# Kernel optimization log

Hardware: AMD Instinct MI355X
Metric: run time of the kernel (lower is better)

The kernel has to match this reference:

```python
import jax, jax.numpy as jnp
import numpy as np
import math

DIM = 256
B, S = 4, 2048


def setup_inputs() -> dict:
    key = jax.random.key(0)
    ks = jax.random.split(key, 8)
    h = DIM // 2
    return {
        "features": jax.random.normal(ks[0], (B, S, DIM), dtype=jnp.float32),
        "W1": jax.random.normal(ks[1], (DIM, h), dtype=jnp.float32) / np.sqrt(DIM),
        "b1": jnp.zeros((h,), dtype=jnp.float32),
        "ln_g": jnp.ones((h,), dtype=jnp.float32),
        "ln_b": jnp.zeros((h,), dtype=jnp.float32),
        "W2": jax.random.normal(ks[2], (h, 1), dtype=jnp.float32) / np.sqrt(h),
        "b2": jnp.zeros((1,), dtype=jnp.float32),
        "target_entropy": jnp.full((1,), math.log(DIM), dtype=jnp.float32),
        "temperature": jnp.ones((1,), dtype=jnp.float32),
    }


def _compute_entropy(features, temperature):
    b, s, d = features.shape
    x = features.reshape(-1, d)  # [N, D]
    sq = jnp.sum(x * x, axis=-1)  # [N]
    # squared euclidean distance (cdist(...)**2), clamped for numerical safety
    d2 = jnp.maximum(sq[:, None] + sq[None, :] - 2.0 * (x @ x.T), 0.0)  # [N, N]
    kernel = jnp.exp(-d2 / (2.0 * temperature[0] ** 2))
    probs = kernel / jnp.sum(kernel, axis=-1, keepdims=True)
    entropy = -jnp.sum(probs * jnp.log(probs + 1e-6), axis=-1)
    return entropy.reshape(b, s)


def _entropy_estimator(features, W1, b1, ln_g, ln_b, W2, b2):
    h = features @ W1 + b1  # [B, S, D/2]
    mu = jnp.mean(h, axis=-1, keepdims=True)
    var = jnp.mean((h - mu) ** 2, axis=-1, keepdims=True)
    hn = (h - mu) / jnp.sqrt(var + 1e-5) * ln_g + ln_b
    hg = jax.nn.gelu(hn, approximate=False)
    return (hg @ W2 + b2).squeeze(-1)  # [B, S]


def reference(features, W1, b1, ln_g, ln_b, W2, b2, target_entropy, temperature):
    current_entropy = _compute_entropy(features, temperature)  # [B, S]
    # estimated_entropy is computed in the original forward but unused in outputs
    _est = _entropy_estimator(features, W1, b1, ln_g, ln_b, W2, b2)
    entropy_diff = current_entropy - target_entropy[0]
    control_signal = jax.nn.sigmoid(-entropy_diff / temperature[0])  # [B, S]
    controlled_features = features * control_signal[..., None]
    return controlled_features, control_signal
```

## Files before the change

### kernel.cpp

```cpp
#include <hip/hip_runtime.h>

#define N 8192
#define D 256
#define BM 128
#define BN 64
#define CH 512
#define NJT (CH / BN)

typedef short short8 __attribute__((ext_vector_type(8)));
typedef float f32x4 __attribute__((ext_vector_type(4)));

__device__ __forceinline__ unsigned short f2bf(float f) {
    unsigned int u = __float_as_uint(f);
    u += 0x7fffu + ((u >> 16) & 1u);
    return (unsigned short)(u >> 16);
}
__device__ __forceinline__ float bf2f(unsigned short h) {
    return __uint_as_float(((unsigned int)h) << 16);
}

#define GLDS16(g, l) __builtin_amdgcn_global_load_lds(                      \
    (const __attribute__((address_space(1))) void*)(g),                     \
    (__attribute__((address_space(3))) void*)(l), 16, 0, 0)

__global__ __launch_bounds__(256) void k_cvt(const float* __restrict__ x,
                                             unsigned short* __restrict__ xb,
                                             float* __restrict__ sq,
                                             float* __restrict__ Sarr,
                                             float* __restrict__ Larr) {
    const int wv = threadIdx.x >> 6, lane = threadIdx.x & 63;
    const int row = blockIdx.x * 4 + wv;
    const float4 v = ((const float4*)x)[(size_t)row * 64 + lane];
    unsigned short pa = f2bf(v.x), pb = f2bf(v.y), pc = f2bf(v.z), pd = f2bf(v.w);
    float a = bf2f(pa), b = bf2f(pb), c = bf2f(pc), d = bf2f(pd);
    float s = a * a + b * b + c * c + d * d;
    ((ushort4*)xb)[(size_t)row * 64 + lane] = make_ushort4(pa, pb, pc, pd);
#pragma unroll
    for (int m = 1; m < 64; m <<= 1) s += __shfl_xor(s, m, 64);
    if (lane == 0) {
        sq[row] = s;
        Sarr[row] = 0.0f;
        Larr[row] = 0.0f;
    }
}

__global__ __launch_bounds__(256, 3) void k_gram(const unsigned short* __restrict__ xb,
                                                 const float* __restrict__ sq,
                                                 const float* __restrict__ temp,
                                                 float* __restrict__ Sarr,
                                                 float* __restrict__ Larr) {
    __shared__ unsigned short Bs[BN * D];

    const int tid = threadIdx.x;
    const int wv = tid >> 6, lane = tid & 63;
    const int q = lane >> 4, c = lane & 15;
    const int rowbase = blockIdx.x * BM;
    const int colbase0 = blockIdx.y * CH;
    const float T = temp[0];
    const float inv2T2 = 1.0f / (2.0f * T * T);

    short8 av[2][8];
#pragma unroll
    for (int tr = 0; tr < 2; ++tr) {
        const unsigned short* ap = xb + (size_t)(rowbase + wv * 32 + tr * 16 + c) * D;
#pragma unroll
        for (int kk = 0; kk < 8; ++kk)
            av[tr][kk] = *(const short8*)(ap + kk * 32 + q * 8);
    }

    float sqr[8];
#pragma unroll
    for (int tr = 0; tr < 2; ++tr)
#pragma unroll
        for (int r = 0; r < 4; ++r)
            sqr[tr * 4 + r] = sq[rowbase + wv * 32 + tr * 16 + q * 4 + r];

    int rofs[4], rx3[4];
#pragma unroll
    for (int tc = 0; tc < 4; ++tc) {
        int r = tc * 16 + c;
        rofs[tc] = r * D;
        rx3[tc] = r & 7;
    }

    const int seg0 = wv * 8;
    const int rhalf = lane >> 5, slot = lane & 31;

    float Sp[8], Lp[8];
#pragma unroll
    for (int i = 0; i < 8; ++i) { Sp[i] = 0.0f; Lp[i] = 0.0f; }

    for (int jt = 0; jt < NJT; ++jt) {
        const int colbase = colbase0 + jt * BN;
        __syncthreads();
#pragma unroll
        for (int i = 0; i < 8; ++i) {
            int seg = seg0 + i;
            int row = seg * 2 + rhalf;
            int g = slot ^ (row & 7);
            GLDS16(xb + (size_t)(colbase + row) * D + g * 8, Bs + seg * 512);
        }
        __syncthreads();

        f32x4 acc[2][4];
#pragma unroll
        for (int tr = 0; tr < 2; ++tr)
#pragma unroll
            for (int tc = 0; tc < 4; ++tc)
#pragma unroll
                for (int r = 0; r < 4; ++r) acc[tr][tc][r] = 0.0f;

#pragma unroll
        for (int kk = 0; kk < 8; ++kk) {
            short8 bv[4];
#pragma unroll
            for (int tc = 0; tc < 4; ++tc)
                bv[tc] = *(const short8*)(Bs + rofs[tc] + (((4 * kk + q) ^ rx3[tc]) << 3));
#pragma unroll
            for (int tr = 0; tr < 2; ++tr)
#pragma unroll
                for (int tc = 0; tc < 4; ++tc)
                    acc[tr][tc] = __builtin_amdgcn_mfma_f32_16x16x32_bf16(
                        av[tr][kk], bv[tc], acc[tr][tc], 0, 0, 0);
        }

        float scq[4];
#pragma unroll
        for (int tc = 0; tc < 4; ++tc) scq[tc] = sq[colbase + tc * 16 + c];

#pragma unroll
        for (int tr = 0; tr < 2; ++tr)
#pragma unroll
            for (int tc = 0; tc < 4; ++tc)
#pragma unroll
                for (int r = 0; r < 4; ++r) {
                    float g = acc[tr][tc][r];
                    float d2 = fmaxf(sqr[tr * 4 + r] + scq[tc] - 2.0f * g, 0.0f);
                    float t = -d2 * inv2T2;
                    float e = __expf(t);
                    Sp[tr * 4 + r] += e;
                    Lp[tr * 4 + r] += e * t;
                }
    }

#pragma unroll
    for (int m = 1; m <= 8; m <<= 1)
#pragma unroll
        for (int i = 0; i < 8; ++i) {
            Sp[i] += __shfl_xor(Sp[i], m, 64);
            Lp[i] += __shfl_xor(Lp[i], m, 64);
        }
    if (c == 0) {
#pragma unroll
        for (int i = 0; i < 8; ++i) {
            int row = rowbase + wv * 32 + (i >> 2) * 16 + q * 4 + (i & 3);
            atomicAdd(&Sarr[row], Sp[i]);
            atomicAdd(&Larr[row], Lp[i]);
        }
    }
}

__global__ __launch_bounds__(256) void k_ctrl(const float* __restrict__ Sarr,
                                              const float* __restrict__ Larr,
                                              const float* __restrict__ target,
                                              const float* __restrict__ temp,
                                              float* __restrict__ ctrl,
                                              float* __restrict__ out) {
    const int r = blockIdx.x * 256 + threadIdx.x;
    float S = Sarr[r], L = Larr[r];
    float H = __logf(S) - L / S;
    float z = (H - target[0]) / temp[0];
    float cs = 1.0f / (1.0f + __expf(z));
    ctrl[r] = cs;
    out[(size_t)N * D + r] = cs;
}

__global__ __launch_bounds__(256) void k_scale(const float* __restrict__ x,
                                               const float* __restrict__ ctrl,
                                               float* __restrict__ out) {
    const size_t i = (size_t)blockIdx.x * 256 + threadIdx.x;
    float4 v = ((const float4*)x)[i];
    float cs = ctrl[i >> 6];
    float4 o;
    o.x = v.x * cs; o.y = v.y * cs; o.z = v.z * cs; o.w = v.w * cs;
    ((float4*)out)[i] = o;
}

extern "C" void kernel_launch(void* const* d_in, const int* in_sizes, int n_in,
                              void* d_out, int out_size, void* d_ws, size_t ws_size,
                              hipStream_t stream) {
    const float* x = (const float*)d_in[0];
    const float* target = (const float*)d_in[7];
    const float* temp = (const float*)d_in[8];
    float* out = (float*)d_out;

    float* wsf = (float*)d_ws;
    float* sq = wsf;
    float* Sarr = wsf + N;
    float* Larr = wsf + 2 * N;
    float* ctrl = wsf + 3 * N;

    const size_t need = 4 * (size_t)N * sizeof(float) + (size_t)N * D * sizeof(unsigned short);
    unsigned short* xb = (ws_size >= need) ? (unsigned short*)(wsf + 4 * N)
                                           : (unsigned short*)d_out;

    k_cvt<<<N / 4, 256, 0, stream>>>(x, xb, sq, Sarr, Larr);
    k_gram<<<dim3(N / BM, N / CH), 256, 0, stream>>>(xb, sq, temp, Sarr, Larr);
    k_ctrl<<<N / 256, 256, 0, stream>>>(Sarr, Larr, target, temp, ctrl, out);
    k_scale<<<(N * (D / 4)) / 256, 256, 0, stream>>>(x, ctrl, out);
}
```

Before: 126.1 us.

## Exploit Gram matrix symmetry with upper-triangular tiles and fuse control/scale kernels

Uses the symmetry of the pairwise distance matrix by launching only the upper-triangular 128x128 tile pairs (2080 blocks). Each exp value is accumulated into both the row and the column entropy sums, with column sums sent via extra atomics. This roughly halves the MFMA and exp work, at the cost of more registers, lower occupancy (launch bounds go from 3 to 2) and extra atomic traffic. The control and scale kernels are also merged into one, so the ctrl buffer and one launch go away.

```diff
diff --git a/kernel.cpp b/kernel.cpp
--- a/kernel.cpp
+++ b/kernel.cpp
@@ -3,9 +3,6 @@
 #define N 8192
 #define D 256
 #define BM 128
-#define BN 64
-#define CH 512
-#define NJT (CH / BN)
 
 typedef short short8 __attribute__((ext_vector_type(8)));
 typedef float f32x4 __attribute__((ext_vector_type(4)));
@@ -44,64 +41,65 @@
     }
 }
 
-__global__ __launch_bounds__(256, 3) void k_gram(const unsigned short* __restrict__ xb,
+__global__ __launch_bounds__(256, 2) void k_gram(const unsigned short* __restrict__ xb,
                                                  const float* __restrict__ sq,
                                                  const float* __restrict__ temp,
                                                  float* __restrict__ Sarr,
                                                  float* __restrict__ Larr) {
-    __shared__ unsigned short Bs[BN * D];
+    __shared__ unsigned short Bs[BM * D];
 
     const int tid = threadIdx.x;
     const int wv = tid >> 6, lane = tid & 63;
-    const int q = lane >> 4, c = lane & 15;
-    const int rowbase = blockIdx.x * BM;
-    const int colbase0 = blockIdx.y * CH;
+    const int q8 = lane >> 4, c = lane & 15;
+
+    const int b = blockIdx.x;
+    int p = (int)((129.0f - sqrtf(16641.0f - 8.0f * (float)b)) * 0.5f);
+    while (64 * p - (p * (p - 1)) / 2 > b) --p;
+    while (64 * (p + 1) - ((p + 1) * p) / 2 <= b) ++p;
+    const int qblk = p + (b - (64 * p - (p * (p - 1)) / 2));
+    const int rowbase = p * BM, colbase = qblk * BM;
+
+    const int rhalf = lane >> 5, slot = lane & 31;
+#pragma unroll
+    for (int i = 0; i < 16; ++i) {
+        int seg = wv * 16 + i;
+        int row = seg * 2 + rhalf;
+        int g = slot ^ (row & 7);
+        GLDS16(xb + (size_t)(colbase + row) * D + g * 8, Bs + seg * 512);
+    }
+
+    short8 av[2][8];
+#pragma unroll
+    for (int tr = 0; tr < 2; ++tr) {
+        const unsigned short* ap = xb + (size_t)(rowbase + wv * 32 + tr * 16 + c) * D;
+#pragma unroll
+        for (int kk = 0; kk < 8; ++kk)
+            av[tr][kk] = *(const short8*)(ap + kk * 32 + q8 * 8);
+    }
+
+    float sqr[8];
+#pragma unroll
+    for (int tr = 0; tr < 2; ++tr)
+#pragma unroll
+        for (int r = 0; r < 4; ++r)
+            sqr[tr * 4 + r] = sq[rowbase + wv * 32 + tr * 16 + q8 * 4 + r];
+    float scq[8];
+#pragma unroll
+    for (int i = 0; i < 8; ++i)
+        scq[i] = sq[colbase + (i >> 2) * 64 + (i & 3) * 16 + c];
+
     const float T = temp[0];
     const float inv2T2 = 1.0f / (2.0f * T * T);
-
-    short8 av[2][8];
-#pragma unroll
-    for (int tr = 0; tr < 2; ++tr) {
-        const unsigned short* ap = xb + (size_t)(rowbase + wv * 32 + tr * 16 + c) * D;
-#pragma unroll
-        for (int kk = 0; kk < 8; ++kk)
-            av[tr][kk] = *(const short8*)(ap + kk * 32 + q * 8);
-    }
-
-    float sqr[8];
-#pragma unroll
-    for (int tr = 0; tr < 2; ++tr)
-#pragma unroll
-        for (int r = 0; r < 4; ++r)
-            sqr[tr * 4 + r] = sq[rowbase + wv * 32 + tr * 16 + q * 4 + r];
-
-    int rofs[4], rx3[4];
-#pragma unroll
-    for (int tc = 0; tc < 4; ++tc) {
-        int r = tc * 16 + c;
-        rofs[tc] = r * D;
-        rx3[tc] = r & 7;
-    }
-
-    const int seg0 = wv * 8;
-    const int rhalf = lane >> 5, slot = lane & 31;
-
-    float Sp[8], Lp[8];
-#pragma unroll
-    for (int i = 0; i < 8; ++i) { Sp[i] = 0.0f; Lp[i] = 0.0f; }
-
-    for (int jt = 0; jt < NJT; ++jt) {
-        const int colbase = colbase0 + jt * BN;
-        __syncthreads();
-#pragma unroll
-        for (int i = 0; i < 8; ++i) {
-            int seg = seg0 + i;
-            int row = seg * 2 + rhalf;
-            int g = slot ^ (row & 7);
-            GLDS16(xb + (size_t)(colbase + row) * D + g * 8, Bs + seg * 512);
-        }
-        __syncthreads();
-
+    const int rx = c & 7;
+
+    float Sr[8], Mr[8], Sc[8], Mc[8];
+#pragma unroll
+    for (int i = 0; i < 8; ++i) { Sr[i] = 0.f; Mr[i] = 0.f; Sc[i] = 0.f; Mc[i] = 0.f; }
+
+    __syncthreads();
+
+#pragma unroll
+    for (int jt = 0; jt < 2; ++jt) {
         f32x4 acc[2][4];
 #pragma unroll
         for (int tr = 0; tr < 2; ++tr)
@@ -115,7 +113,8 @@
             short8 bv[4];
 #pragma unroll
             for (int tc = 0; tc < 4; ++tc)
-                bv[tc] = *(const short8*)(Bs + rofs[tc] + (((4 * kk + q) ^ rx3[tc]) << 3));
+                bv[tc] = *(const short8*)(Bs + (jt * 64 + tc * 16 + c) * D +
+                                          (((4 * kk + q8) ^ rx) << 3));
 #pragma unroll
             for (int tr = 0; tr < 2; ++tr)
 #pragma unroll
@@ -124,10 +123,6 @@
                         av[tr][kk], bv[tc], acc[tr][tc], 0, 0, 0);
         }
 
-        float scq[4];
-#pragma unroll
-        for (int tc = 0; tc < 4; ++tc) scq[tc] = sq[colbase + tc * 16 + c];
-
 #pragma unroll
         for (int tr = 0; tr < 2; ++tr)
 #pragma unroll
@@ -135,11 +130,13 @@
 #pragma unroll
                 for (int r = 0; r < 4; ++r) {
                     float g = acc[tr][tc][r];
-                    float d2 = fmaxf(sqr[tr * 4 + r] + scq[tc] - 2.0f * g, 0.0f);
+                    float d2 = fmaxf(sqr[tr * 4 + r] + scq[jt * 4 + tc] - 2.0f * g, 0.0f);
                     float t = -d2 * inv2T2;
                     float e = __expf(t);
-                    Sp[tr * 4 + r] += e;
-                    Lp[tr * 4 + r] += e * t;
+                    Sr[tr * 4 + r] += e;
+                    Mr[tr * 4 + r] = fmaf(e, t, Mr[tr * 4 + r]);
+                    Sc[jt * 4 + tc] += e;
+                    Mc[jt * 4 + tc] = fmaf(e, t, Mc[jt * 4 + tc]);
                 }
     }
 
@@ -147,43 +144,54 @@
     for (int m = 1; m <= 8; m <<= 1)
 #pragma unroll
         for (int i = 0; i < 8; ++i) {
-            Sp[i] += __shfl_xor(Sp[i], m, 64);
-            Lp[i] += __shfl_xor(Lp[i], m, 64);
+            Sr[i] += __shfl_xor(Sr[i], m, 64);
+            Mr[i] += __shfl_xor(Mr[i], m, 64);
         }
     if (c == 0) {
 #pragma unroll
         for (int i = 0; i < 8; ++i) {
-            int row = rowbase + wv * 32 + (i >> 2) * 16 + q * 4 + (i & 3);
-            atomicAdd(&Sarr[row], Sp[i]);
-            atomicAdd(&Larr[row], Lp[i]);
-        }
-    }
-}
-
-__global__ __launch_bounds__(256) void k_ctrl(const float* __restrict__ Sarr,
-                                              const float* __restrict__ Larr,
-                                              const float* __restrict__ target,
-                                              const float* __restrict__ temp,
-                                              float* __restrict__ ctrl,
-                                              float* __restrict__ out) {
-    const int r = blockIdx.x * 256 + threadIdx.x;
-    float S = Sarr[r], L = Larr[r];
+            int row = rowbase + wv * 32 + (i >> 2) * 16 + q8 * 4 + (i & 3);
+            atomicAdd(&Sarr[row], Sr[i]);
+            atomicAdd(&Larr[row], Mr[i]);
+        }
+    }
+
+    if (p != qblk) {
+#pragma unroll
+        for (int m = 16; m <= 32; m <<= 1)
+#pragma unroll
+            for (int i = 0; i < 8; ++i) {
+                Sc[i] += __shfl_xor(Sc[i], m, 64);
+                Mc[i] += __shfl_xor(Mc[i], m, 64);
+            }
+        if (q8 == 0) {
+#pragma unroll
+            for (int i = 0; i < 8; ++i) {
+                int col = colbase + (i >> 2) * 64 + (i & 3) * 16 + c;
+                atomicAdd(&Sarr[col], Sc[i]);
+                atomicAdd(&Larr[col], Mc[i]);
+            }
+        }
+    }
+}
+
+__global__ __launch_bounds__(256) void k_finish(const float* __restrict__ x,
+                                                const float* __restrict__ Sarr,
+                                                const float* __restrict__ Larr,
+                                                const float* __restrict__ target,
+                                                const float* __restrict__ temp,
+                                                float* __restrict__ out) {
+    const int gid = blockIdx.x * 256 + threadIdx.x;
+    const int row = gid >> 6;
+    float S = Sarr[row], L = Larr[row];
     float H = __logf(S) - L / S;
     float z = (H - target[0]) / temp[0];
     float cs = 1.0f / (1.0f + __expf(z));
-    ctrl[r] = cs;
-    out[(size_t)N * D + r] = cs;
-}
-
-__global__ __launch_bounds__(256) void k_scale(const float* __restrict__ x,
-                                               const float* __restrict__ ctrl,
-                                               float* __restrict__ out) {
-    const size_t i = (size_t)blockIdx.x * 256 + threadIdx.x;
-    float4 v = ((const float4*)x)[i];
-    float cs = ctrl[i >> 6];
+    float4 v = ((const float4*)x)[gid];
     float4 o;
     o.x = v.x * cs; o.y = v.y * cs; o.z = v.z * cs; o.w = v.w * cs;
-    ((float4*)out)[i] = o;
+    ((float4*)out)[gid] = o;
+    if ((gid & 63) == 0) out[(size_t)N * D + row] = cs;
 }
 
 extern "C" void kernel_launch(void* const* d_in, const int* in_sizes, int n_in,
@@ -198,14 +206,12 @@
     float* sq = wsf;
     float* Sarr = wsf + N;
     float* Larr = wsf + 2 * N;
-    float* ctrl = wsf + 3 * N;
-
-    const size_t need = 4 * (size_t)N * sizeof(float) + (size_t)N * D * sizeof(unsigned short);
-    unsigned short* xb = (ws_size >= need) ? (unsigned short*)(wsf + 4 * N)
+
+    const size_t need = 3 * (size_t)N * sizeof(float) + (size_t)N * D * sizeof(unsigned short);
+    unsigned short* xb = (ws_size >= need) ? (unsigned short*)(wsf + 3 * N)
                                            : (unsigned short*)d_out;
 
     k_cvt<<<N / 4, 256, 0, stream>>>(x, xb, sq, Sarr, Larr);
-    k_gram<<<dim3(N / BM, N / CH), 256, 0, stream>>>(xb, sq, temp, Sarr, Larr);
-    k_ctrl<<<N / 256, 256, 0, stream>>>(Sarr, Larr, target, temp, ctrl, out);
-    k_scale<<<(N * (D / 4)) / 256, 256, 0, stream>>>(x, ctrl, out);
-}
+    k_gram<<<2080, 256, 0, stream>>>(xb, sq, temp, Sarr, Larr);
+    k_finish<<<(N * (D / 4)) / 256, 256, 0, stream>>>(x, Sarr, Larr, target, temp, out);
+}
```

New measurement: 137.0 us. 1.09x slower.
